# Kernel tuning notes

Hardware: AMD Instinct MI355X
Metric: run time of the kernel (lower is better)

Reference implementation:

```python
import jax, jax.numpy as jnp
import numpy as np

B, C, N, K = 8, 64, 4096, 16


def setup_inputs() -> dict:
    key = jax.random.key(0)
    k1, k2 = jax.random.split(key)
    x = jax.random.normal(k1, (B, C, N, 1), dtype=jnp.float32)
    edge_index = jax.random.randint(k2, (B, N, K), 0, N, dtype=jnp.int32)
    alpha = jnp.float32(1.0)  # AlphaLayer parameter, init 1.0
    return {"x": x, "edge_index": edge_index, "alpha": alpha}


def _aggregate_sum(x_nodes, edge_index):
    # x_nodes: [B, N, C]; edge_index: [B, N, K] neighbor ids per node.
    b, n, c = x_nodes.shape
    k = edge_index.shape[-1]
    idx = edge_index.reshape(b, n * k, 1).astype(jnp.int32)
    gathered = jnp.take_along_axis(x_nodes, idx, axis=1)  # [B, N*K, C]
    return gathered.reshape(b, n, k, c).sum(axis=2)       # [B, N, C]


def reference(x, edge_index, alpha):
    # x: [B, C, N, 1] -> permute(0,2,3,1) -> [B, N, 1, C]; W=1 so treat as [B, N, C]
    x_nodes = jnp.transpose(x[..., 0], (0, 2, 1))          # [B, N, C]
    m = _aggregate_sum(x_nodes, edge_index)                # [B, N, C]
    m = jnp.transpose(m, (0, 2, 1))[..., None]             # back to [B, C, N, 1]
    # AlphaLayer: x * (1 + alpha) + m
    return x * (1.0 + alpha) + m
```

## Files before the change

kernel.cpp:

```cpp
#include <hip/hip_runtime.h>

#define B_ 8
#define C_ 64
#define N_ 4096
#define K_ 16
#define THREADS 1024
#define CG 8
#define NQ 4

typedef __fp16 half2_t __attribute__((ext_vector_type(2)));

__device__ __forceinline__ unsigned pkrtz(float lo, float hi) {
  half2_t h = __builtin_amdgcn_cvt_pkrtz(lo, hi);
  unsigned u; __builtin_memcpy(&u, &h, 4);
  return u;
}
__device__ __forceinline__ half2_t as_h2(unsigned u) {
  half2_t h; __builtin_memcpy(&h, &u, 4);
  return h;
}

__global__ __launch_bounds__(THREADS) void fused_k(const float* __restrict__ x,
                                                   const int* __restrict__ ei,
                                                   const float* __restrict__ alpha_p,
                                                   float* __restrict__ out) {
  __shared__ uint4 xs[N_];
  const int bid = blockIdx.x;
  const int b   = bid & 7;
  const int cg  = (bid >> 3) & 7;
  const int nq  = bid >> 6;
  const int c0  = cg * CG;
  const int t   = threadIdx.x;

  const float* xb = x + ((size_t)b * C_ + c0) * N_;

  const int node = nq * (N_ / NQ) + t;
  const int4* ep = reinterpret_cast<const int4*>(ei + ((size_t)b * N_ + node) * K_);
  const int4 e0 = ep[0], e1 = ep[1], e2 = ep[2], e3 = ep[3];

#pragma unroll
  for (int p = 0; p < N_ / THREADS; ++p) {
    const int n = p * THREADS + t;
    float r[CG];
#pragma unroll
    for (int c = 0; c < CG; ++c) r[c] = xb[c * N_ + n];
    uint4 w;
    w.x = pkrtz(r[0], r[1]);
    w.y = pkrtz(r[2], r[3]);
    w.z = pkrtz(r[4], r[5]);
    w.w = pkrtz(r[6], r[7]);
    xs[n] = w;
  }
  __syncthreads();

  int idx[K_];
  *reinterpret_cast<int4*>(&idx[0])  = e0;
  *reinterpret_cast<int4*>(&idx[4])  = e1;
  *reinterpret_cast<int4*>(&idx[8])  = e2;
  *reinterpret_cast<int4*>(&idx[12]) = e3;

  half2_t a0 = {0, 0}, a1 = {0, 0}, a2 = {0, 0}, a3 = {0, 0};
#pragma unroll
  for (int k = 0; k < K_; ++k) {
    const uint4 v = xs[idx[k]];
    a0 += as_h2(v.x);
    a1 += as_h2(v.y);
    a2 += as_h2(v.z);
    a3 += as_h2(v.w);
  }

  float acc[CG];
  acc[0] = (float)a0[0]; acc[1] = (float)a0[1];
  acc[2] = (float)a1[0]; acc[3] = (float)a1[1];
  acc[4] = (float)a2[0]; acc[5] = (float)a2[1];
  acc[6] = (float)a3[0]; acc[7] = (float)a3[1];

  const float s = 1.0f + alpha_p[0];
  float* ob = out + ((size_t)b * C_ + c0) * N_;
#pragma unroll
  for (int c = 0; c < CG; ++c) {
    ob[c * N_ + node] = xb[c * N_ + node] * s + acc[c];
  }
}

extern "C" void kernel_launch(void* const* d_in, const int* in_sizes, int n_in,
                              void* d_out, int out_size, void* d_ws, size_t ws_size,
                              hipStream_t stream) {
  const float* x     = (const float*)d_in[0];
  const int*   ei    = (const int*)d_in[1];
  const float* alpha = (const float*)d_in[2];
  float*       out   = (float*)d_out;
  (void)d_ws; (void)ws_size;

  fused_k<<<B_ * (C_ / CG) * NQ, THREADS, 0, stream>>>(x, ei, alpha, out);
}
```

Before: 11.09 us.

## Split channel group into two phases to overlap second load with first gather

Splits the 8-channel shared-memory tile into two 4-channel halves. The second half's global loads are issued before the first half's gather-sum and stored after it, so load latency overlaps LDS gather work. The self term is now read from the fp16 shared copy instead of re-reading fp32 x from global memory. This removes a global read but lowers the precision of the x*(1+alpha) term and adds a second barrier.

```diff
diff --git a/kernel.cpp b/kernel.cpp
--- a/kernel.cpp
+++ b/kernel.cpp
@@ -5,7 +5,6 @@
 #define N_ 4096
 #define K_ 16
 #define THREADS 1024
-#define CG 8
 #define NQ 4
 
 typedef __fp16 half2_t __attribute__((ext_vector_type(2)));
@@ -24,15 +23,17 @@
                                                    const int* __restrict__ ei,
                                                    const float* __restrict__ alpha_p,
                                                    float* __restrict__ out) {
-  __shared__ uint4 xs[N_];
+  __shared__ uint2 xsA[N_];
+  __shared__ uint2 xsB[N_];
   const int bid = blockIdx.x;
   const int b   = bid & 7;
   const int cg  = (bid >> 3) & 7;
   const int nq  = bid >> 6;
-  const int c0  = cg * CG;
+  const int c0  = cg * 8;
   const int t   = threadIdx.x;
 
-  const float* xb = x + ((size_t)b * C_ + c0) * N_;
+  const float* xbA = x + ((size_t)b * C_ + c0) * N_;
+  const float* xbB = xbA + 4 * N_;
 
   const int node = nq * (N_ / NQ) + t;
   const int4* ep = reinterpret_cast<const int4*>(ei + ((size_t)b * N_ + node) * K_);
@@ -41,15 +42,10 @@
 #pragma unroll
   for (int p = 0; p < N_ / THREADS; ++p) {
     const int n = p * THREADS + t;
-    float r[CG];
-#pragma unroll
-    for (int c = 0; c < CG; ++c) r[c] = xb[c * N_ + n];
-    uint4 w;
-    w.x = pkrtz(r[0], r[1]);
-    w.y = pkrtz(r[2], r[3]);
-    w.z = pkrtz(r[4], r[5]);
-    w.w = pkrtz(r[6], r[7]);
-    xs[n] = w;
+    const float r0 = xbA[0 * N_ + n], r1 = xbA[1 * N_ + n];
+    const float r2 = xbA[2 * N_ + n], r3 = xbA[3 * N_ + n];
+    uint2 w; w.x = pkrtz(r0, r1); w.y = pkrtz(r2, r3);
+    xsA[n] = w;
   }
   __syncthreads();
 
@@ -59,27 +55,56 @@
   *reinterpret_cast<int4*>(&idx[8])  = e2;
   *reinterpret_cast<int4*>(&idx[12]) = e3;
 
-  half2_t a0 = {0, 0}, a1 = {0, 0}, a2 = {0, 0}, a3 = {0, 0};
+  float rb[N_ / THREADS][4];
+#pragma unroll
+  for (int p = 0; p < N_ / THREADS; ++p) {
+    const int n = p * THREADS + t;
+#pragma unroll
+    for (int c = 0; c < 4; ++c) rb[p][c] = xbB[c * N_ + n];
+  }
+
+  half2_t a0 = {0, 0}, a1 = {0, 0};
 #pragma unroll
   for (int k = 0; k < K_; ++k) {
-    const uint4 v = xs[idx[k]];
+    const uint2 v = xsA[idx[k]];
     a0 += as_h2(v.x);
     a1 += as_h2(v.y);
-    a2 += as_h2(v.z);
-    a3 += as_h2(v.w);
+  }
+  const uint2 svA = xsA[node];
+
+  const float s = 1.0f + alpha_p[0];
+  float* obA = out + ((size_t)b * C_ + c0) * N_;
+  {
+    const half2_t s0 = as_h2(svA.x), s1 = as_h2(svA.y);
+    obA[0 * N_ + node] = (float)s0[0] * s + (float)a0[0];
+    obA[1 * N_ + node] = (float)s0[1] * s + (float)a0[1];
+    obA[2 * N_ + node] = (float)s1[0] * s + (float)a1[0];
+    obA[3 * N_ + node] = (float)s1[1] * s + (float)a1[1];
   }
 
-  float acc[CG];
-  acc[0] = (float)a0[0]; acc[1] = (float)a0[1];
-  acc[2] = (float)a1[0]; acc[3] = (float)a1[1];
-  acc[4] = (float)a2[0]; acc[5] = (float)a2[1];
-  acc[6] = (float)a3[0]; acc[7] = (float)a3[1];
+#pragma unroll
+  for (int p = 0; p < N_ / THREADS; ++p) {
+    const int n = p * THREADS + t;
+    uint2 w; w.x = pkrtz(rb[p][0], rb[p][1]); w.y = pkrtz(rb[p][2], rb[p][3]);
+    xsB[n] = w;
+  }
+  __syncthreads();
 
-  const float s = 1.0f + alpha_p[0];
-  float* ob = out + ((size_t)b * C_ + c0) * N_;
+  half2_t b0 = {0, 0}, b1 = {0, 0};
 #pragma unroll
-  for (int c = 0; c < CG; ++c) {
-    ob[c * N_ + node] = xb[c * N_ + node] * s + acc[c];
+  for (int k = 0; k < K_; ++k) {
+    const uint2 v = xsB[idx[k]];
+    b0 += as_h2(v.x);
+    b1 += as_h2(v.y);
+  }
+  const uint2 svB = xsB[node];
+  float* obB = obA + 4 * N_;
+  {
+    const half2_t s0 = as_h2(svB.x), s1 = as_h2(svB.y);
+    obB[0 * N_ + node] = (float)s0[0] * s + (float)b0[0];
+    obB[1 * N_ + node] = (float)s0[1] * s + (float)b0[1];
+    obB[2 * N_ + node] = (float)s1[0] * s + (float)b1[0];
+    obB[3 * N_ + node] = (float)s1[1] * s + (float)b1[1];
   }
 }
 
@@ -92,5 +117,5 @@
   float*       out   = (float*)d_out;
   (void)d_ws; (void)ws_size;
 
-  fused_k<<<B_ * (C_ / CG) * NQ, THREADS, 0, stream>>>(x, ei, alpha, out);
+  fused_k<<<B_ * 8 * NQ, THREADS, 0, stream>>>(x, ei, alpha, out);
 }
```

New measurement: 11.05 us. Within noise of the previous version (-0.3%).
